# Kernel optimization log

Measured on AMD Instinct MI355X. Metric: run time of the kernel, lower is better.

## Reference

```python
import jax, jax.numpy as jnp
import numpy as np

N_NODES = 100000
N_EDGES = 1600000
N_GRAPHS = 128
DIM = 64
N_LAYERS = 4
DENSE = 256
BN_EPS = 1e-5


def setup_inputs() -> dict:
    key = jax.random.key(0)
    ks = list(jax.random.split(key, 24))
    k = iter(ks)
    def lin(kk, fan_in, shape):
        b = 1.0 / np.sqrt(fan_in)
        return jax.random.uniform(kk, shape, jnp.float32, -b, b)
    inp = {}
    inp['x'] = jax.random.normal(next(k), (N_NODES, 32), jnp.float32)
    inp['edge_attr'] = jax.random.normal(next(k), (N_EDGES, 16), jnp.float32)
    inp['edge_index'] = jax.random.randint(next(k), (2, N_EDGES), 0, N_NODES, jnp.int32)
    inp['batch'] = jnp.sort(jax.random.randint(next(k), (N_NODES,), 0, N_GRAPHS, jnp.int32))
    # encoders
    inp['node_W'] = lin(next(k), 32, (32, DIM)); inp['node_b'] = lin(next(k), 32, (DIM,))
    inp['edge_W'] = lin(next(k), 16, (16, DIM)); inp['edge_b'] = lin(next(k), 16, (DIM,))
    # per-layer GINE MLPs (stacked over layer dim) and BN affine params
    inp['mlp1_W'] = lin(next(k), DIM, (N_LAYERS, DIM, DIM)); inp['mlp1_b'] = lin(next(k), DIM, (N_LAYERS, DIM))
    inp['mlp2_W'] = lin(next(k), DIM, (N_LAYERS, DIM, DIM)); inp['mlp2_b'] = lin(next(k), DIM, (N_LAYERS, DIM))
    inp['bn_gamma'] = jnp.ones((N_LAYERS, DIM), jnp.float32)
    inp['bn_beta'] = jnp.zeros((N_LAYERS, DIM), jnp.float32)
    # head: Linear(128,256) -> Linear(256,128) -> Linear(128,1)
    inp['head1_W'] = lin(next(k), 2 * DIM, (2 * DIM, DENSE)); inp['head1_b'] = lin(next(k), 2 * DIM, (DENSE,))
    inp['head2_W'] = lin(next(k), DENSE, (DENSE, DENSE // 2)); inp['head2_b'] = lin(next(k), DENSE, (DENSE // 2,))
    inp['head3_W'] = lin(next(k), DENSE // 2, (DENSE // 2, 1)); inp['head3_b'] = lin(next(k), DENSE // 2, (1,))
    return inp


def reference(x, edge_attr, edge_index, batch, node_W, node_b, edge_W, edge_b,
              mlp1_W, mlp1_b, mlp2_W, mlp2_b, bn_gamma, bn_beta,
              head1_W, head1_b, head2_W, head2_b, head3_W, head3_b):
    src, dst = edge_index[0], edge_index[1]  # messages flow src (x_j) -> dst (x_i)
    h = x @ node_W + node_b                  # [N, DIM]
    e = edge_attr @ edge_W + edge_b          # [E, DIM]
    for l in range(N_LAYERS):
        # GINEConv (eps = 0, not trained): mlp((1+eps)*x_i + sum_j relu(x_j + e_ij))
        msg = jax.nn.relu(h[src] + e)                              # [E, DIM]
        agg = jax.ops.segment_sum(msg, dst, num_segments=N_NODES)  # [N, DIM]
        z = h + agg
        z = jax.nn.relu(z @ mlp1_W[l] + mlp1_b[l]) @ mlp2_W[l] + mlp2_b[l]
        # BatchNorm1d (training-mode batch statistics, biased variance)
        mu = jnp.mean(z, axis=0)
        var = jnp.mean(jnp.square(z - mu), axis=0)
        z = (z - mu) * jax.lax.rsqrt(var + BN_EPS) * bn_gamma[l] + bn_beta[l]
        h = jax.nn.relu(z)
    sums = jax.ops.segment_sum(h, batch, num_segments=N_GRAPHS)                      # [G, DIM]
    counts = jax.ops.segment_sum(jnp.ones((h.shape[0],), h.dtype), batch, num_segments=N_GRAPHS)
    means = sums / jnp.maximum(counts, 1.0)[:, None]
    g = jnp.concatenate([sums, means], axis=1)   # [G, 2*DIM]
    g = jax.nn.relu(g @ head1_W + head1_b)       # dropout is identity at inference
    g = jax.nn.relu(g @ head2_W + head2_b)
    logits = (g @ head3_W + head3_b).reshape(-1) # [G]
    return logits
```

## Files before the change

### kernel.cpp

```cpp
#include <hip/hip_runtime.h>

#define SCAN_B 1024
#define NGRAPH 128
typedef unsigned short u16;
typedef unsigned int u32;
typedef u32 u32x2 __attribute__((ext_vector_type(2)));
typedef u32 u32x4 __attribute__((ext_vector_type(4)));
typedef _Float16 f16;
typedef _Float16 f16x2 __attribute__((ext_vector_type(2)));
typedef _Float16 f16x8 __attribute__((ext_vector_type(8)));
typedef float f32x4 __attribute__((ext_vector_type(4)));

__device__ __forceinline__ u16 f2h(float f) {
  f16 h = (f16)f;
  return __builtin_bit_cast(u16, h);
}
__device__ __forceinline__ float h2f(u16 u) {
  return (float)__builtin_bit_cast(f16, u);
}
__device__ __forceinline__ float hlo(u32 w) { return h2f((u16)(w & 0xffffu)); }
__device__ __forceinline__ float hhi(u32 w) { return h2f((u16)(w >> 16)); }

__global__ __launch_bounds__(256) void node_enc_kernel(
    const float* __restrict__ x, const float* __restrict__ W,
    const float* __restrict__ b, u16* __restrict__ zh, int N)
{
  int lane = threadIdx.x & 63;
  int wave = (blockIdx.x * blockDim.x + threadIdx.x) >> 6;
  int nw = (gridDim.x * blockDim.x) >> 6;
  float wcol[32];
#pragma unroll
  for (int k = 0; k < 32; ++k) wcol[k] = W[k * 64 + lane];
  float bb = b[lane];
  for (int n = wave; n < N; n += nw) {
    const float4* xr = (const float4*)(x + (size_t)n * 32);
    float acc = bb;
#pragma unroll
    for (int c = 0; c < 8; ++c) {
      float4 v = xr[c];
      acc = fmaf(v.x, wcol[4 * c + 0], acc);
      acc = fmaf(v.y, wcol[4 * c + 1], acc);
      acc = fmaf(v.z, wcol[4 * c + 2], acc);
      acc = fmaf(v.w, wcol[4 * c + 3], acc);
    }
    zh[(size_t)n * 64 + lane] = f2h(acc);
  }
}

__global__ __launch_bounds__(256) void count_pos_kernel(
    const int* __restrict__ dst, int* __restrict__ deg,
    int* __restrict__ pos, int E)
{
  int e = blockIdx.x * blockDim.x + threadIdx.x;
  if (e < E) pos[e] = atomicAdd(&deg[dst[e]], 1);
}

__global__ __launch_bounds__(SCAN_B) void scan1_kernel(
    const int* __restrict__ deg, int* __restrict__ rowp,
    int* __restrict__ bsum, int N)
{
  __shared__ int s[SCAN_B];
  int tid = threadIdx.x;
  int i = blockIdx.x * SCAN_B + tid;
  int v = (i < N) ? deg[i] : 0;
  s[tid] = v;
  __syncthreads();
  for (int off = 1; off < SCAN_B; off <<= 1) {
    int t = (tid >= off) ? s[tid - off] : 0;
    __syncthreads();
    s[tid] += t;
    __syncthreads();
  }
  if (i < N) rowp[i] = s[tid] - v;
  if (tid == SCAN_B - 1) bsum[blockIdx.x] = s[tid];
}

__global__ __launch_bounds__(128) void scan2_kernel(int* __restrict__ bsum, int NB)
{
  __shared__ int s[128];
  int tid = threadIdx.x;
  int v = (tid < NB) ? bsum[tid] : 0;
  s[tid] = v;
  __syncthreads();
  for (int off = 1; off < 128; off <<= 1) {
    int t = (tid >= off) ? s[tid - off] : 0;
    __syncthreads();
    s[tid] += t;
    __syncthreads();
  }
  if (tid < NB) bsum[tid] = s[tid] - v;
}

__global__ __launch_bounds__(SCAN_B) void scan3_kernel(
    int* __restrict__ rowp, const int* __restrict__ bsum, int N, int E)
{
  int i = blockIdx.x * SCAN_B + threadIdx.x;
  if (i < N) rowp[i] += bsum[blockIdx.x];
  if (i == 0) rowp[N] = E;
}

__global__ __launch_bounds__(256) void scatter_pos_kernel(
    const int* __restrict__ dst, const int* __restrict__ rowp,
    const int* __restrict__ pos, int* __restrict__ eids, int E)
{
  int e = blockIdx.x * blockDim.x + threadIdx.x;
  if (e >= E) return;
  int p = rowp[dst[e]] + pos[e];
  eids[p] = e;
}

__global__ __launch_bounds__(256) void scatter_e_kernel(
    const int* __restrict__ dst, const int* __restrict__ src,
    const int* __restrict__ pos, const float4* __restrict__ attr4,
    const int* __restrict__ rowp, const float* __restrict__ eW,
    const float* __restrict__ eb_, int* __restrict__ src_s,
    u16* __restrict__ e_s, int E)
{
  int lane = threadIdx.x & 63;
  int c = lane & 15, q = lane >> 4;
  int wave = (blockIdx.x * blockDim.x + threadIdx.x) >> 6;
  int base = wave << 6;
  if (base >= E) return;
  int nb = E - base; if (nb > 64) nb = 64;

  float wcol[4][16];
#pragma unroll
  for (int ch = 0; ch < 4; ++ch)
#pragma unroll
    for (int k = 0; k < 16; ++k)
      wcol[ch][k] = eW[k * 64 + 4 * c + ch];
  float4 eb4 = *(const float4*)&eb_[4 * c];

  int pv = 0;
  if (lane < nb) {
    int e = base + lane;
    pv = rowp[dst[e]] + pos[e];
    src_s[pv] = src[e];
  }

  auto enc = [&](float4 a0, float4 a1, float4 a2, float4 a3, int slot) {
    float m0 = eb4.x, m1 = eb4.y, m2 = eb4.z, m3 = eb4.w;
#define ESTEP(av, k)                                                   \
    m0 = fmaf(av, wcol[0][k], m0); m1 = fmaf(av, wcol[1][k], m1);      \
    m2 = fmaf(av, wcol[2][k], m2); m3 = fmaf(av, wcol[3][k], m3);
    ESTEP(a0.x, 0)  ESTEP(a0.y, 1)  ESTEP(a0.z, 2)  ESTEP(a0.w, 3)
    ESTEP(a1.x, 4)  ESTEP(a1.y, 5)  ESTEP(a1.z, 6)  ESTEP(a1.w, 7)
    ESTEP(a2.x, 8)  ESTEP(a2.y, 9)  ESTEP(a2.z, 10) ESTEP(a2.w, 11)
    ESTEP(a3.x, 12) ESTEP(a3.y, 13) ESTEP(a3.z, 14) ESTEP(a3.w, 15)
#undef ESTEP
    u32x2 o;
    o[0] = (u32)f2h(m0) | ((u32)f2h(m1) << 16);
    o[1] = (u32)f2h(m2) | ((u32)f2h(m3) << 16);
    *(u32x2*)(e_s + (size_t)slot * 64 + 4 * c) = o;
  };

  if (nb == 64) {
#pragma unroll 2
    for (int t = 0; t < 16; t += 2) {
      int pA = __shfl(pv, 4 * t + q, 64);
      int pB = __shfl(pv, 4 * t + 4 + q, 64);
      const float4* rA = attr4 + (size_t)(base + 4 * t + q) * 4;
      const float4* rB = attr4 + (size_t)(base + 4 * t + 4 + q) * 4;
      float4 A0 = rA[0], A1 = rA[1], A2 = rA[2], A3 = rA[3];
      float4 B0 = rB[0], B1 = rB[1], B2 = rB[2], B3 = rB[3];
      enc(A0, A1, A2, A3, pA);
      enc(B0, B1, B2, B3, pB);
    }
  } else {
    for (int t = 0; 4 * t < nb; ++t) {
      int idx = 4 * t + q;
      int p = __shfl(pv, idx < nb ? idx : 0, 64);
      if (idx < nb) {
        const float4* rA = attr4 + (size_t)(base + idx) * 4;
        float4 A0 = rA[0], A1 = rA[1], A2 = rA[2], A3 = rA[3];
        enc(A0, A1, A2, A3, p);
      }
    }
  }
}

__global__ __launch_bounds__(256) void prep_weights_kernel(
    const float* __restrict__ mlp1_W, const float* __restrict__ mlp2_W,
    u16* __restrict__ Wt)
{
  int idx = blockIdx.x * 256 + threadIdx.x;
  if (idx >= 32768) return;
  int layer = idx >> 13;
  int which = (idx >> 12) & 1;
  int d = (idx >> 6) & 63;
  int k = idx & 63;
  const float* W = which ? mlp2_W : mlp1_W;
  Wt[idx] = f2h(W[layer * 4096 + k * 64 + d]);
}

__global__ __launch_bounds__(256, 4) void gather_kernel(
    const u16* __restrict__ zh, const float* __restrict__ scsh,
    const u16* __restrict__ e_s, const int* __restrict__ srcv,
    const int* __restrict__ rowp, u16* __restrict__ gh, int N, int use_bn)
{
  int lane = threadIdx.x & 63;
  int c = lane & 15, q = lane >> 4;
  int wave = (blockIdx.x * blockDim.x + threadIdx.x) >> 6;
  int nw = (gridDim.x * blockDim.x) >> 6;

  float4 sc4 = make_float4(1.f, 1.f, 1.f, 1.f);
  float4 sh4 = make_float4(0.f, 0.f, 0.f, 0.f);
  if (use_bn) {
    sc4 = *(const float4*)&scsh[4 * c];
    sh4 = *(const float4*)&scsh[64 + 4 * c];
  }

  auto hval4 = [&](u32x2 z, float& h0, float& h1, float& h2, float& h3) {
    h0 = hlo(z[0]); h1 = hhi(z[0]); h2 = hlo(z[1]); h3 = hhi(z[1]);
    if (use_bn) {
      h0 = fmaxf(fmaf(h0, sc4.x, sh4.x), 0.f);
      h1 = fmaxf(fmaf(h1, sc4.y, sh4.y), 0.f);
      h2 = fmaxf(fmaf(h2, sc4.z, sh4.z), 0.f);
      h3 = fmaxf(fmaf(h3, sc4.w, sh4.w), 0.f);
    }
  };
  auto body = [&](u32x2 z, u32x2 e,
                  float& A0, float& A1, float& A2, float& A3) {
    float h0, h1, h2, h3;
    hval4(z, h0, h1, h2, h3);
    A0 += fmaxf(h0 + hlo(e[0]), 0.f);
    A1 += fmaxf(h1 + hhi(e[0]), 0.f);
    A2 += fmaxf(h2 + hlo(e[1]), 0.f);
    A3 += fmaxf(h3 + hhi(e[1]), 0.f);
  };

  for (int node = wave; node < N; node += nw) {
    const int j0 = rowp[node], j1 = rowp[node + 1];
    float acc0 = 0.f, acc1 = 0.f, acc2 = 0.f, acc3 = 0.f;

    for (int base = j0; base < j1; base += 64) {
      int nb = j1 - base; if (nb > 64) nb = 64;
      int iv = (lane < nb) ? srcv[base + lane] : 0;
      int ng = nb >> 2;
      int t = 0;
      for (; t + 4 <= ng; t += 4) {
        int s0 = __shfl(iv, 4 * t + q, 64);
        int s1 = __shfl(iv, 4 * t + 4 + q, 64);
        int s2 = __shfl(iv, 4 * t + 8 + q, 64);
        int s3 = __shfl(iv, 4 * t + 12 + q, 64);
        u32x2 z0 = *(const u32x2*)(zh + (size_t)s0 * 64 + 4 * c);
        u32x2 z1 = *(const u32x2*)(zh + (size_t)s1 * 64 + 4 * c);
        u32x2 z2 = *(const u32x2*)(zh + (size_t)s2 * 64 + 4 * c);
        u32x2 z3 = *(const u32x2*)(zh + (size_t)s3 * 64 + 4 * c);
        u32x2 e0 = *(const u32x2*)(e_s + (size_t)(base + 4 * t + q) * 64 + 4 * c);
        u32x2 e1 = *(const u32x2*)(e_s + (size_t)(base + 4 * t + 4 + q) * 64 + 4 * c);
        u32x2 e2 = *(const u32x2*)(e_s + (size_t)(base + 4 * t + 8 + q) * 64 + 4 * c);
        u32x2 e3 = *(const u32x2*)(e_s + (size_t)(base + 4 * t + 12 + q) * 64 + 4 * c);
        body(z0, e0, acc0, acc1, acc2, acc3);
        body(z1, e1, acc0, acc1, acc2, acc3);
        body(z2, e2, acc0, acc1, acc2, acc3);
        body(z3, e3, acc0, acc1, acc2, acc3);
      }
      for (; t < ng; ++t) {
        int s0 = __shfl(iv, 4 * t + q, 64);
        u32x2 z0 = *(const u32x2*)(zh + (size_t)s0 * 64 + 4 * c);
        u32x2 e0 = *(const u32x2*)(e_s + (size_t)(base + 4 * t + q) * 64 + 4 * c);
        body(z0, e0, acc0, acc1, acc2, acc3);
      }
      int tail = nb & 3;
      if (tail) {
        int idx = 4 * ng + (q < tail ? q : 0);
        int s0 = __shfl(iv, idx, 64);
        u32x2 z0 = *(const u32x2*)(zh + (size_t)s0 * 64 + 4 * c);
        u32x2 e0 = *(const u32x2*)(e_s + (size_t)(base + idx) * 64 + 4 * c);
        float h0, h1, h2, h3;
        hval4(z0, h0, h1, h2, h3);
        float wmask = (q < tail) ? 1.f : 0.f;
        acc0 += wmask * fmaxf(h0 + hlo(e0[0]), 0.f);
        acc1 += wmask * fmaxf(h1 + hhi(e0[0]), 0.f);
        acc2 += wmask * fmaxf(h2 + hlo(e0[1]), 0.f);
        acc3 += wmask * fmaxf(h3 + hhi(e0[1]), 0.f);
      }
    }
    acc0 += __shfl_xor(acc0, 16, 64); acc0 += __shfl_xor(acc0, 32, 64);
    acc1 += __shfl_xor(acc1, 16, 64); acc1 += __shfl_xor(acc1, 32, 64);
    acc2 += __shfl_xor(acc2, 16, 64); acc2 += __shfl_xor(acc2, 32, 64);
    acc3 += __shfl_xor(acc3, 16, 64); acc3 += __shfl_xor(acc3, 32, 64);
    if (q == 0) {
      u32x2 zn = *(const u32x2*)(zh + (size_t)node * 64 + 4 * c);
      float h0, h1, h2, h3;
      hval4(zn, h0, h1, h2, h3);
      acc0 += h0; acc1 += h1; acc2 += h2; acc3 += h3;
      u32x2 o;
      o[0] = (u32)f2h(acc0) | ((u32)f2h(acc1) << 16);
      o[1] = (u32)f2h(acc2) | ((u32)f2h(acc3) << 16);
      *(u32x2*)(gh + (size_t)node * 64 + 4 * c) = o;
    }
  }
}

__global__ __launch_bounds__(256) void gather_fallback_kernel(
    const u16* __restrict__ zh, const float* __restrict__ scsh,
    const int* __restrict__ srcv, const int* __restrict__ eids,
    const int* __restrict__ rowp, const float* __restrict__ attr,
    const float* __restrict__ eW, const float* __restrict__ eb_,
    u16* __restrict__ gh, int N, int use_bn)
{
  int lane = threadIdx.x & 63;
  int node = (blockIdx.x * blockDim.x + threadIdx.x) >> 6;
  if (node >= N) return;
  float sc = 1.f, sh = 0.f;
  if (use_bn) { sc = scsh[lane]; sh = scsh[64 + lane]; }
  auto hval = [&](float zz) -> float {
    float v = fmaf(zz, sc, sh);
    return use_bn ? fmaxf(v, 0.f) : v;
  };
  float wcol[16];
#pragma unroll
  for (int k = 0; k < 16; ++k) wcol[k] = eW[k * 64 + lane];
  float eb = eb_[lane];
  const int j0 = rowp[node], j1 = rowp[node + 1];
  float acc = hval(h2f(zh[(size_t)node * 64 + lane]));
  for (int j = j0; j < j1; ++j) {
    int eid = eids[j];
    int s = srcv[j];
    const float4* ar = (const float4*)(attr + (size_t)eid * 16);
    float4 a0 = ar[0], a1 = ar[1], a2 = ar[2], a3 = ar[3];
    float m = eb;
    m = fmaf(a0.x, wcol[0], m);  m = fmaf(a0.y, wcol[1], m);
    m = fmaf(a0.z, wcol[2], m);  m = fmaf(a0.w, wcol[3], m);
    m = fmaf(a1.x, wcol[4], m);  m = fmaf(a1.y, wcol[5], m);
    m = fmaf(a1.z, wcol[6], m);  m = fmaf(a1.w, wcol[7], m);
    m = fmaf(a2.x, wcol[8], m);  m = fmaf(a2.y, wcol[9], m);
    m = fmaf(a2.z, wcol[10], m); m = fmaf(a2.w, wcol[11], m);
    m = fmaf(a3.x, wcol[12], m); m = fmaf(a3.y, wcol[13], m);
    m = fmaf(a3.z, wcol[14], m); m = fmaf(a3.w, wcol[15], m);
    acc += fmaxf(hval(h2f(zh[(size_t)s * 64 + lane])) + m, 0.f);
  }
  gh[(size_t)node * 64 + lane] = f2h(acc);
}

__global__ __launch_bounds__(256) void mlp_mfma_kernel(
    const u16* __restrict__ gh, u16* __restrict__ zh,
    const u16* __restrict__ W1t, const u16* __restrict__ W2t,
    const float* __restrict__ b1, const float* __restrict__ b2,
    float* __restrict__ stat, int N)
{
  __shared__ __align__(16) u16 ylds[4][16][72];
  __shared__ float sstat[128];
  int tid = threadIdx.x, lane = tid & 63, w = tid >> 6;
  int l15 = lane & 15, lg = lane >> 4;
  int row_base = (blockIdx.x * 4 + w) * 32;

  if (tid < 128) sstat[tid] = 0.f;
  __syncthreads();

  f16x8 w1f[2][4], w2f[2][4];
#pragma unroll
  for (int ks = 0; ks < 2; ++ks)
#pragma unroll
    for (int nt = 0; nt < 4; ++nt) {
      int off = (nt * 16 + l15) * 64 + ks * 32 + lg * 8;
      w1f[ks][nt] = *(const f16x8*)&W1t[off];
      w2f[ks][nt] = *(const f16x8*)&W2t[off];
    }
  float bv1[4], bv2[4];
#pragma unroll
  for (int nt = 0; nt < 4; ++nt) {
    bv1[nt] = b1[nt * 16 + l15];
    bv2[nt] = b2[nt * 16 + l15];
  }

  float s1acc[4] = {0.f, 0.f, 0.f, 0.f};
  float s2acc[4] = {0.f, 0.f, 0.f, 0.f};

#pragma unroll
  for (int tile = 0; tile < 2; ++tile) {
    int grow0 = row_base + tile * 16;
    int arow = grow0 + l15; if (arow >= N) arow = N - 1;
    const u16* grow = gh + (size_t)arow * 64;
    f16x8 a0 = *(const f16x8*)(grow + lg * 8);
    f16x8 a1 = *(const f16x8*)(grow + 32 + lg * 8);

    f32x4 c1[4];
#pragma unroll
    for (int nt = 0; nt < 4; ++nt) {
      c1[nt] = (f32x4){0.f, 0.f, 0.f, 0.f};
      c1[nt] = __builtin_amdgcn_mfma_f32_16x16x32_f16(a0, w1f[0][nt], c1[nt], 0, 0, 0);
      c1[nt] = __builtin_amdgcn_mfma_f32_16x16x32_f16(a1, w1f[1][nt], c1[nt], 0, 0, 0);
    }
#pragma unroll
    for (int nt = 0; nt < 4; ++nt)
#pragma unroll
      for (int r = 0; r < 4; ++r)
        ylds[w][lg * 4 + r][nt * 16 + l15] = f2h(fmaxf(c1[nt][r] + bv1[nt], 0.f));
    f16x8 a20 = *(const f16x8*)&ylds[w][l15][lg * 8];
    f16x8 a21 = *(const f16x8*)&ylds[w][l15][32 + lg * 8];

    f32x4 c2[4];
#pragma unroll
    for (int nt = 0; nt < 4; ++nt) {
      c2[nt] = (f32x4){0.f, 0.f, 0.f, 0.f};
      c2[nt] = __builtin_amdgcn_mfma_f32_16x16x32_f16(a20, w2f[0][nt], c2[nt], 0, 0, 0);
      c2[nt] = __builtin_amdgcn_mfma_f32_16x16x32_f16(a21, w2f[1][nt], c2[nt], 0, 0, 0);
    }
#pragma unroll
    for (int nt = 0; nt < 4; ++nt) {
#pragma unroll
      for (int r = 0; r < 4; ++r) {
        int row = grow0 + lg * 4 + r;
        float v = c2[nt][r] + bv2[nt];
        bool ok = row < N;
        if (ok) zh[(size_t)row * 64 + nt * 16 + l15] = f2h(v);
        float vm = ok ? v : 0.f;
        s1acc[nt] += vm;
        s2acc[nt] = fmaf(vm, vm, s2acc[nt]);
      }
    }
  }

#pragma unroll
  for (int nt = 0; nt < 4; ++nt) {
    float s1 = s1acc[nt], s2 = s2acc[nt];
    s1 += __shfl_xor(s1, 16, 64); s1 += __shfl_xor(s1, 32, 64);
    s2 += __shfl_xor(s2, 16, 64); s2 += __shfl_xor(s2, 32, 64);
    if (lg == 0) {
      atomicAdd(&sstat[nt * 16 + l15], s1);
      atomicAdd(&sstat[64 + nt * 16 + l15], s2);
    }
  }
  __syncthreads();
  if (tid < 128) atomicAdd(&stat[tid], sstat[tid]);
}

__global__ __launch_bounds__(64) void bnfinal_kernel(
    const float* __restrict__ stat, const float* __restrict__ gamma,
    const float* __restrict__ beta, float* __restrict__ scsh, float invN)
{
  int d = threadIdx.x;
  float mu = stat[d] * invN;
  float var = stat[64 + d] * invN - mu * mu;
  var = fmaxf(var, 0.f);
  float sc = gamma[d] * rsqrtf(var + 1e-5f);
  scsh[d] = sc;
  scsh[64 + d] = beta[d] - mu * sc;
}

__global__ __launch_bounds__(256) void pool_kernel(
    const u16* __restrict__ zh, const float* __restrict__ scsh,
    const int* __restrict__ batch,
    float* __restrict__ sums, float* __restrict__ cnts, int N)
{
  int lane = threadIdx.x & 63;
  int wave = (blockIdx.x * blockDim.x + threadIdx.x) >> 6;
  int r0 = wave * 64;
  if (r0 >= N) return;
  float sc = scsh[lane], sh = scsh[64 + lane];
  int r1 = min(r0 + 64, N);
  int cur = batch[r0];
  float acc = 0.f;
  int cnt = 0;
  for (int r = r0; r < r1; ++r) {
    int bg = batch[r];
    if (bg != cur) {
      atomicAdd(&sums[(size_t)cur * 64 + lane], acc);
      if (lane == 0) atomicAdd(&cnts[cur], (float)cnt);
      acc = 0.f; cnt = 0; cur = bg;
    }
    acc += fmaxf(fmaf(h2f(zh[(size_t)r * 64 + lane]), sc, sh), 0.f);
    cnt++;
  }
  atomicAdd(&sums[(size_t)cur * 64 + lane], acc);
  if (lane == 0) atomicAdd(&cnts[cur], (float)cnt);
}

__global__ __launch_bounds__(256) void head_kernel(
    const float* __restrict__ sums, const float* __restrict__ cnts,
    const float* __restrict__ W1, const float* __restrict__ b1,
    const float* __restrict__ W2, const float* __restrict__ b2,
    const float* __restrict__ W3, const float* __restrict__ b3,
    float* __restrict__ out)
{
  __shared__ float gf[128];
  __shared__ float h1s[256];
  __shared__ float h2s[128];
  int g = blockIdx.x, t = threadIdx.x;
  if (t < 64) {
    float sv = sums[(size_t)g * 64 + t];
    gf[t] = sv;
    gf[64 + t] = sv / fmaxf(cnts[g], 1.f);
  }
  __syncthreads();
  float a = b1[t];
  for (int k = 0; k < 128; ++k) a = fmaf(gf[k], W1[k * 256 + t], a);
  h1s[t] = fmaxf(a, 0.f);
  __syncthreads();
  if (t < 128) {
    float a2 = b2[t];
    for (int k = 0; k < 256; ++k) a2 = fmaf(h1s[k], W2[k * 128 + t], a2);
    h2s[t] = fmaxf(a2, 0.f);
  }
  __syncthreads();
  if (t == 0) {
    float s = b3[0];
    for (int k = 0; k < 128; ++k) s = fmaf(h2s[k], W3[k], s);
    out[g] = s;
  }
}

extern "C" void kernel_launch(void* const* d_in, const int* in_sizes, int n_in,
                              void* d_out, int out_size, void* d_ws, size_t ws_size,
                              hipStream_t stream)
{
  const float* x         = (const float*)d_in[0];
  const float* edge_attr = (const float*)d_in[1];
  const int*   ei        = (const int*)  d_in[2];
  const int*   batch     = (const int*)  d_in[3];
  const float* node_W    = (const float*)d_in[4];
  const float* node_b    = (const float*)d_in[5];
  const float* edge_W    = (const float*)d_in[6];
  const float* edge_b    = (const float*)d_in[7];
  const float* mlp1_W    = (const float*)d_in[8];
  const float* mlp1_b    = (const float*)d_in[9];
  const float* mlp2_W    = (const float*)d_in[10];
  const float* mlp2_b    = (const float*)d_in[11];
  const float* bn_gamma  = (const float*)d_in[12];
  const float* bn_beta   = (const float*)d_in[13];
  const float* head1_W   = (const float*)d_in[14];
  const float* head1_b   = (const float*)d_in[15];
  const float* head2_W   = (const float*)d_in[16];
  const float* head2_b   = (const float*)d_in[17];
  const float* head3_W   = (const float*)d_in[18];
  const float* head3_b   = (const float*)d_in[19];
  float* out = (float*)d_out;
  (void)n_in; (void)out_size;

  const int N = in_sizes[0] / 32;
  const int E = in_sizes[2] / 2;
  const int* srcp = ei;
  const int* dstp = ei + E;

  auto al = [](size_t b) { return (b + 255) & ~(size_t)255; };
  const size_t sz_zh   = al((size_t)N * 64 * 2);
  const size_t sz_g    = al((size_t)N * 64 * 2);
  const size_t sz_es   = al((size_t)E * 64 * 2);
  const size_t sz_src  = al((size_t)E * 4);
  const size_t sz_pos  = al((size_t)E * 4);
  const size_t sz_eids = al((size_t)E * 4);
  const size_t sz_rowp = al((size_t)(N + 1) * 4);
  const size_t sz_wt   = al(32768 * 2);
  const size_t sz_scr  = al((size_t)N * 4);
  const size_t sz_small = al(512) * 3 + al(NGRAPH * 64 * 4) + al(NGRAPH * 4);

  const size_t need_sorted = sz_zh + sz_g + sz_es + sz_src + sz_pos +
                             sz_eids + sz_rowp + sz_wt + sz_scr + sz_small;
  const bool sorted = ws_size >= need_sorted;

  char* p = (char*)d_ws;
  auto take = [&](size_t b) -> char* { char* q = p; p += b; return q; };

  u16*   zh   = (u16*)  take(sz_zh);
  u16*   gh   = (u16*)  take(sz_g);
  int*   rowp = (int*)  take(sz_rowp);
  u16*   Wt   = (u16*)  take(sz_wt);
  float* stat = (float*)take(al(512));
  float* scsh = (float*)take(al(512));
  int*   bsum = (int*)  take(al(512));
  float* sums = (float*)take(al(NGRAPH * 64 * 4));
  float* cnts = (float*)take(al(NGRAPH * 4));
  int*   deg  = (int*)  take(sz_scr);
  int*   pos  = (int*)  take(sz_pos);
  int*   eids = (int*)  take(sz_eids);
  int*   src_s= (int*)  take(sz_src);

  u16* e_s = nullptr;
  if (sorted) e_s = (u16*)take(sz_es);

  const int NB = (N + SCAN_B - 1) / SCAN_B;

  hipMemsetAsync(deg, 0, (size_t)N * 4, stream);

  node_enc_kernel<<<2048, 256, 0, stream>>>(x, node_W, node_b, zh, N);
  prep_weights_kernel<<<128, 256, 0, stream>>>(mlp1_W, mlp2_W, Wt);
  count_pos_kernel<<<(E + 255) / 256, 256, 0, stream>>>(dstp, deg, pos, E);
  scan1_kernel<<<NB, SCAN_B, 0, stream>>>(deg, rowp, bsum, N);
  scan2_kernel<<<1, 128, 0, stream>>>(bsum, NB);
  scan3_kernel<<<NB, SCAN_B, 0, stream>>>(rowp, bsum, N, E);
  if (sorted) {
    scatter_e_kernel<<<(E + 255) / 256, 256, 0, stream>>>(
        dstp, srcp, pos, (const float4*)edge_attr, rowp, edge_W, edge_b,
        src_s, e_s, E);
  } else {
    scatter_pos_kernel<<<(E + 255) / 256, 256, 0, stream>>>(
        dstp, rowp, pos, eids, E);
    scatter_e_kernel<<<(E + 255) / 256, 256, 0, stream>>>(
        dstp, srcp, pos, (const float4*)edge_attr, rowp, edge_W, edge_b,
        src_s, nullptr, E);
  }

  const int mlpBlocks = (N + 127) / 128;
  for (int l = 0; l < 4; ++l) {
    if (sorted) {
      gather_kernel<<<4096, 256, 0, stream>>>(
          zh, scsh, e_s, src_s, rowp, gh, N, l > 0);
    } else {
      gather_fallback_kernel<<<(N + 3) / 4, 256, 0, stream>>>(
          zh, scsh, src_s, eids, rowp, edge_attr, edge_W, edge_b, gh, N, l > 0);
    }
    hipMemsetAsync(stat, 0, 512, stream);
    mlp_mfma_kernel<<<mlpBlocks, 256, 0, stream>>>(
        gh, zh, Wt + (size_t)l * 8192, Wt + (size_t)l * 8192 + 4096,
        mlp1_b + (size_t)l * 64, mlp2_b + (size_t)l * 64, stat, N);
    bnfinal_kernel<<<1, 64, 0, stream>>>(
        stat, bn_gamma + (size_t)l * 64, bn_beta + (size_t)l * 64, scsh,
        1.0f / (float)N);
  }

  hipMemsetAsync(sums, 0, (size_t)NGRAPH * 64 * 4, stream);
  hipMemsetAsync(cnts, 0, (size_t)NGRAPH * 4, stream);
  const int poolWaves = (N + 63) / 64;
  pool_kernel<<<(poolWaves + 3) / 4, 256, 0, stream>>>(zh, scsh, batch, sums, cnts, N);
  head_kernel<<<NGRAPH, 256, 0, stream>>>(
      sums, cnts, head1_W, head1_b, head2_W, head2_b, head3_W, head3_b, out);
}
```

Baseline: 743.8 us.

## Fold BN finalize into consumers and zero stats in gather; nontemporal input loads

Removes the separate per-layer bnfinal kernel and stat memset by having each consumer kernel (gather, fallback gather, pool) compute BN scale and shift directly from the raw sum statistics. It double-buffers the stat arrays, and block 0 of the gather zeroes the buffer the following MLP accumulates into. It also switches the streaming reads of x and edge_attr to nontemporal loads. This saves two small launches per layer at the cost of redundant per-wave rsqrt work.

```diff
diff --git a/kernel.cpp b/kernel.cpp
--- a/kernel.cpp
+++ b/kernel.cpp
@@ -6,6 +6,7 @@
 typedef unsigned int u32;
 typedef u32 u32x2 __attribute__((ext_vector_type(2)));
 typedef u32 u32x4 __attribute__((ext_vector_type(4)));
+typedef float fx4 __attribute__((ext_vector_type(4)));
 typedef _Float16 f16;
 typedef _Float16 f16x2 __attribute__((ext_vector_type(2)));
 typedef _Float16 f16x8 __attribute__((ext_vector_type(8)));
@@ -21,6 +22,25 @@
 __device__ __forceinline__ float hlo(u32 w) { return h2f((u16)(w & 0xffffu)); }
 __device__ __forceinline__ float hhi(u32 w) { return h2f((u16)(w >> 16)); }
 
+__device__ __forceinline__ void bn4(const float* __restrict__ stat,
+                                    const float* __restrict__ gamma,
+                                    const float* __restrict__ beta,
+                                    float invN, int c4,
+                                    float4& sc4, float4& sh4)
+{
+  float4 s1 = *(const float4*)&stat[c4];
+  float4 s2 = *(const float4*)&stat[64 + c4];
+  float4 g4 = *(const float4*)&gamma[c4];
+  float4 b4 = *(const float4*)&beta[c4];
+#define BN1(k)                                                        \
+  { float mu = s1.k * invN;                                           \
+    float var = fmaxf(s2.k * invN - mu * mu, 0.f);                    \
+    sc4.k = g4.k * rsqrtf(var + 1e-5f);                               \
+    sh4.k = b4.k - mu * sc4.k; }
+  BN1(x) BN1(y) BN1(z) BN1(w)
+#undef BN1
+}
+
 __global__ __launch_bounds__(256) void node_enc_kernel(
     const float* __restrict__ x, const float* __restrict__ W,
     const float* __restrict__ b, u16* __restrict__ zh, int N)
@@ -33,15 +53,15 @@
   for (int k = 0; k < 32; ++k) wcol[k] = W[k * 64 + lane];
   float bb = b[lane];
   for (int n = wave; n < N; n += nw) {
-    const float4* xr = (const float4*)(x + (size_t)n * 32);
+    const fx4* xr = (const fx4*)(x + (size_t)n * 32);
     float acc = bb;
 #pragma unroll
     for (int c = 0; c < 8; ++c) {
-      float4 v = xr[c];
-      acc = fmaf(v.x, wcol[4 * c + 0], acc);
-      acc = fmaf(v.y, wcol[4 * c + 1], acc);
-      acc = fmaf(v.z, wcol[4 * c + 2], acc);
-      acc = fmaf(v.w, wcol[4 * c + 3], acc);
+      fx4 v = __builtin_nontemporal_load(&xr[c]);
+      acc = fmaf(v[0], wcol[4 * c + 0], acc);
+      acc = fmaf(v[1], wcol[4 * c + 1], acc);
+      acc = fmaf(v[2], wcol[4 * c + 2], acc);
+      acc = fmaf(v[3], wcol[4 * c + 3], acc);
     }
     zh[(size_t)n * 64 + lane] = f2h(acc);
   }
@@ -111,7 +131,7 @@
 
 __global__ __launch_bounds__(256) void scatter_e_kernel(
     const int* __restrict__ dst, const int* __restrict__ src,
-    const int* __restrict__ pos, const float4* __restrict__ attr4,
+    const int* __restrict__ pos, const fx4* __restrict__ attr4,
     const int* __restrict__ rowp, const float* __restrict__ eW,
     const float* __restrict__ eb_, int* __restrict__ src_s,
     u16* __restrict__ e_s, int E)
@@ -138,15 +158,15 @@
     src_s[pv] = src[e];
   }
 
-  auto enc = [&](float4 a0, float4 a1, float4 a2, float4 a3, int slot) {
+  auto enc = [&](fx4 a0, fx4 a1, fx4 a2, fx4 a3, int slot) {
     float m0 = eb4.x, m1 = eb4.y, m2 = eb4.z, m3 = eb4.w;
 #define ESTEP(av, k)                                                   \
     m0 = fmaf(av, wcol[0][k], m0); m1 = fmaf(av, wcol[1][k], m1);      \
     m2 = fmaf(av, wcol[2][k], m2); m3 = fmaf(av, wcol[3][k], m3);
-    ESTEP(a0.x, 0)  ESTEP(a0.y, 1)  ESTEP(a0.z, 2)  ESTEP(a0.w, 3)
-    ESTEP(a1.x, 4)  ESTEP(a1.y, 5)  ESTEP(a1.z, 6)  ESTEP(a1.w, 7)
-    ESTEP(a2.x, 8)  ESTEP(a2.y, 9)  ESTEP(a2.z, 10) ESTEP(a2.w, 11)
-    ESTEP(a3.x, 12) ESTEP(a3.y, 13) ESTEP(a3.z, 14) ESTEP(a3.w, 15)
+    ESTEP(a0[0], 0)  ESTEP(a0[1], 1)  ESTEP(a0[2], 2)  ESTEP(a0[3], 3)
+    ESTEP(a1[0], 4)  ESTEP(a1[1], 5)  ESTEP(a1[2], 6)  ESTEP(a1[3], 7)
+    ESTEP(a2[0], 8)  ESTEP(a2[1], 9)  ESTEP(a2[2], 10) ESTEP(a2[3], 11)
+    ESTEP(a3[0], 12) ESTEP(a3[1], 13) ESTEP(a3[2], 14) ESTEP(a3[3], 15)
 #undef ESTEP
     u32x2 o;
     o[0] = (u32)f2h(m0) | ((u32)f2h(m1) << 16);
@@ -159,10 +179,16 @@
     for (int t = 0; t < 16; t += 2) {
       int pA = __shfl(pv, 4 * t + q, 64);
       int pB = __shfl(pv, 4 * t + 4 + q, 64);
-      const float4* rA = attr4 + (size_t)(base + 4 * t + q) * 4;
-      const float4* rB = attr4 + (size_t)(base + 4 * t + 4 + q) * 4;
-      float4 A0 = rA[0], A1 = rA[1], A2 = rA[2], A3 = rA[3];
-      float4 B0 = rB[0], B1 = rB[1], B2 = rB[2], B3 = rB[3];
+      const fx4* rA = attr4 + (size_t)(base + 4 * t + q) * 4;
+      const fx4* rB = attr4 + (size_t)(base + 4 * t + 4 + q) * 4;
+      fx4 A0 = __builtin_nontemporal_load(rA);
+      fx4 A1 = __builtin_nontemporal_load(rA + 1);
+      fx4 A2 = __builtin_nontemporal_load(rA + 2);
+      fx4 A3 = __builtin_nontemporal_load(rA + 3);
+      fx4 B0 = __builtin_nontemporal_load(rB);
+      fx4 B1 = __builtin_nontemporal_load(rB + 1);
+      fx4 B2 = __builtin_nontemporal_load(rB + 2);
+      fx4 B3 = __builtin_nontemporal_load(rB + 3);
       enc(A0, A1, A2, A3, pA);
       enc(B0, B1, B2, B3, pB);
     }
@@ -171,8 +197,8 @@
       int idx = 4 * t + q;
       int p = __shfl(pv, idx < nb ? idx : 0, 64);
       if (idx < nb) {
-        const float4* rA = attr4 + (size_t)(base + idx) * 4;
-        float4 A0 = rA[0], A1 = rA[1], A2 = rA[2], A3 = rA[3];
+        const fx4* rA = attr4 + (size_t)(base + idx) * 4;
+        fx4 A0 = rA[0], A1 = rA[1], A2 = rA[2], A3 = rA[3];
         enc(A0, A1, A2, A3, p);
       }
     }
@@ -194,25 +220,27 @@
 }
 
 __global__ __launch_bounds__(256, 4) void gather_kernel(
-    const u16* __restrict__ zh, const float* __restrict__ scsh,
+    const u16* __restrict__ zh, const float* __restrict__ stat_rd,
+    const float* __restrict__ gamma, const float* __restrict__ beta,
+    float invN, float* __restrict__ stat_wr,
     const u16* __restrict__ e_s, const int* __restrict__ srcv,
-    const int* __restrict__ rowp, u16* __restrict__ gh, int N, int use_bn)
-{
+    const int* __restrict__ rowp, u16* __restrict__ gh, int N)
+{
+  if (blockIdx.x == 0 && threadIdx.x < 128) stat_wr[threadIdx.x] = 0.f;
+
   int lane = threadIdx.x & 63;
   int c = lane & 15, q = lane >> 4;
   int wave = (blockIdx.x * blockDim.x + threadIdx.x) >> 6;
   int nw = (gridDim.x * blockDim.x) >> 6;
 
+  const bool ubn = stat_rd != nullptr;
   float4 sc4 = make_float4(1.f, 1.f, 1.f, 1.f);
   float4 sh4 = make_float4(0.f, 0.f, 0.f, 0.f);
-  if (use_bn) {
-    sc4 = *(const float4*)&scsh[4 * c];
-    sh4 = *(const float4*)&scsh[64 + 4 * c];
-  }
+  if (ubn) bn4(stat_rd, gamma, beta, invN, 4 * c, sc4, sh4);
 
   auto hval4 = [&](u32x2 z, float& h0, float& h1, float& h2, float& h3) {
     h0 = hlo(z[0]); h1 = hhi(z[0]); h2 = hlo(z[1]); h3 = hhi(z[1]);
-    if (use_bn) {
+    if (ubn) {
       h0 = fmaxf(fmaf(h0, sc4.x, sh4.x), 0.f);
       h1 = fmaxf(fmaf(h1, sc4.y, sh4.y), 0.f);
       h2 = fmaxf(fmaf(h2, sc4.z, sh4.z), 0.f);
@@ -295,20 +323,29 @@
 }
 
 __global__ __launch_bounds__(256) void gather_fallback_kernel(
-    const u16* __restrict__ zh, const float* __restrict__ scsh,
+    const u16* __restrict__ zh, const float* __restrict__ stat_rd,
+    const float* __restrict__ gamma, const float* __restrict__ beta,
+    float invN, float* __restrict__ stat_wr,
     const int* __restrict__ srcv, const int* __restrict__ eids,
     const int* __restrict__ rowp, const float* __restrict__ attr,
     const float* __restrict__ eW, const float* __restrict__ eb_,
-    u16* __restrict__ gh, int N, int use_bn)
-{
+    u16* __restrict__ gh, int N)
+{
+  if (blockIdx.x == 0 && threadIdx.x < 128) stat_wr[threadIdx.x] = 0.f;
   int lane = threadIdx.x & 63;
   int node = (blockIdx.x * blockDim.x + threadIdx.x) >> 6;
   if (node >= N) return;
+  const bool ubn = stat_rd != nullptr;
   float sc = 1.f, sh = 0.f;
-  if (use_bn) { sc = scsh[lane]; sh = scsh[64 + lane]; }
+  if (ubn) {
+    float mu = stat_rd[lane] * invN;
+    float var = fmaxf(stat_rd[64 + lane] * invN - mu * mu, 0.f);
+    sc = gamma[lane] * rsqrtf(var + 1e-5f);
+    sh = beta[lane] - mu * sc;
+  }
   auto hval = [&](float zz) -> float {
     float v = fmaf(zz, sc, sh);
-    return use_bn ? fmaxf(v, 0.f) : v;
+    return ubn ? fmaxf(v, 0.f) : v;
   };
   float wcol[16];
 #pragma unroll
@@ -428,29 +465,20 @@
   if (tid < 128) atomicAdd(&stat[tid], sstat[tid]);
 }
 
-__global__ __launch_bounds__(64) void bnfinal_kernel(
-    const float* __restrict__ stat, const float* __restrict__ gamma,
-    const float* __restrict__ beta, float* __restrict__ scsh, float invN)
-{
-  int d = threadIdx.x;
-  float mu = stat[d] * invN;
-  float var = stat[64 + d] * invN - mu * mu;
-  var = fmaxf(var, 0.f);
-  float sc = gamma[d] * rsqrtf(var + 1e-5f);
-  scsh[d] = sc;
-  scsh[64 + d] = beta[d] - mu * sc;
-}
-
 __global__ __launch_bounds__(256) void pool_kernel(
-    const u16* __restrict__ zh, const float* __restrict__ scsh,
-    const int* __restrict__ batch,
+    const u16* __restrict__ zh, const float* __restrict__ stat_rd,
+    const float* __restrict__ gamma, const float* __restrict__ beta,
+    float invN, const int* __restrict__ batch,
     float* __restrict__ sums, float* __restrict__ cnts, int N)
 {
   int lane = threadIdx.x & 63;
   int wave = (blockIdx.x * blockDim.x + threadIdx.x) >> 6;
   int r0 = wave * 64;
   if (r0 >= N) return;
-  float sc = scsh[lane], sh = scsh[64 + lane];
+  float mu = stat_rd[lane] * invN;
+  float var = fmaxf(stat_rd[64 + lane] * invN - mu * mu, 0.f);
+  float sc = gamma[lane] * rsqrtf(var + 1e-5f);
+  float sh = beta[lane] - mu * sc;
   int r1 = min(r0 + 64, N);
   int cur = batch[r0];
   float acc = 0.f;
@@ -558,8 +586,8 @@
   u16*   gh   = (u16*)  take(sz_g);
   int*   rowp = (int*)  take(sz_rowp);
   u16*   Wt   = (u16*)  take(sz_wt);
-  float* stat = (float*)take(al(512));
-  float* scsh = (float*)take(al(512));
+  float* statA= (float*)take(al(512));
+  float* statB= (float*)take(al(512));
   int*   bsum = (int*)  take(al(512));
   float* sums = (float*)take(al(NGRAPH * 64 * 4));
   float* cnts = (float*)take(al(NGRAPH * 4));
@@ -572,6 +600,8 @@
   if (sorted) e_s = (u16*)take(sz_es);
 
   const int NB = (N + SCAN_B - 1) / SCAN_B;
+  const float invN = 1.0f / (float)N;
+  float* statbuf[2] = {statA, statB};
 
   hipMemsetAsync(deg, 0, (size_t)N * 4, stream);
 
@@ -583,38 +613,41 @@
   scan3_kernel<<<NB, SCAN_B, 0, stream>>>(rowp, bsum, N, E);
   if (sorted) {
     scatter_e_kernel<<<(E + 255) / 256, 256, 0, stream>>>(
-        dstp, srcp, pos, (const float4*)edge_attr, rowp, edge_W, edge_b,
+        dstp, srcp, pos, (const fx4*)edge_attr, rowp, edge_W, edge_b,
         src_s, e_s, E);
   } else {
     scatter_pos_kernel<<<(E + 255) / 256, 256, 0, stream>>>(
         dstp, rowp, pos, eids, E);
     scatter_e_kernel<<<(E + 255) / 256, 256, 0, stream>>>(
-        dstp, srcp, pos, (const float4*)edge_attr, rowp, edge_W, edge_b,
+        dstp, srcp, pos, (const fx4*)edge_attr, rowp, edge_W, edge_b,
         src_s, nullptr, E);
   }
 
   const int mlpBlocks = (N + 127) / 128;
   for (int l = 0; l < 4; ++l) {
+    const float* stat_rd = (l == 0) ? nullptr : statbuf[(l - 1) & 1];
+    float* stat_wr = statbuf[l & 1];
+    const float* gma = bn_gamma + (size_t)(l ? (l - 1) : 0) * 64;
+    const float* bta = bn_beta + (size_t)(l ? (l - 1) : 0) * 64;
     if (sorted) {
       gather_kernel<<<4096, 256, 0, stream>>>(
-          zh, scsh, e_s, src_s, rowp, gh, N, l > 0);
+          zh, stat_rd, gma, bta, invN, stat_wr, e_s, src_s, rowp, gh, N);
     } else {
       gather_fallback_kernel<<<(N + 3) / 4, 256, 0, stream>>>(
-          zh, scsh, src_s, eids, rowp, edge_attr, edge_W, edge_b, gh, N, l > 0);
-    }
-    hipMemsetAsync(stat, 0, 512, stream);
+          zh, stat_rd, gma, bta, invN, stat_wr, src_s, eids, rowp,
+          edge_attr, edge_W, edge_b, gh, N);
+    }
     mlp_mfma_kernel<<<mlpBlocks, 256, 0, stream>>>(
         gh, zh, Wt + (size_t)l * 8192, Wt + (size_t)l * 8192 + 4096,
-        mlp1_b + (size_t)l * 64, mlp2_b + (size_t)l * 64, stat, N);
-    bnfinal_kernel<<<1, 64, 0, stream>>>(
-        stat, bn_gamma + (size_t)l * 64, bn_beta + (size_t)l * 64, scsh,
-        1.0f / (float)N);
+        mlp1_b + (size_t)l * 64, mlp2_b + (size_t)l * 64, stat_wr, N);
   }
 
   hipMemsetAsync(sums, 0, (size_t)NGRAPH * 64 * 4, stream);
   hipMemsetAsync(cnts, 0, (size_t)NGRAPH * 4, stream);
   const int poolWaves = (N + 63) / 64;
-  pool_kernel<<<(poolWaves + 3) / 4, 256, 0, stream>>>(zh, scsh, batch, sums, cnts, N);
+  pool_kernel<<<(poolWaves + 3) / 4, 256, 0, stream>>>(
+      zh, statbuf[1], bn_gamma + 3 * 64, bn_beta + 3 * 64, invN,
+      batch, sums, cnts, N);
   head_kernel<<<NGRAPH, 256, 0, stream>>>(
       sums, cnts, head1_W, head1_b, head2_W, head2_b, head3_W, head3_b, out);
 }
```

After: 739.0 us. About the same (-0.6%).
